# Optimization experiments

Hardware: AMD Instinct MI355X
Metric: run time of the kernel (lower is better)

## Reference

```python
import jax, jax.numpy as jnp
import numpy as np
import math

H, M, N = 64, 128, 128  # volume dims (m == n required by original index math)
K_NEIGH = 9
W_WIN = 3


def build_neighbor_ids(h, n, w):
    # Periodic (wrap-around) neighbor indices, matching extract_neighbour_indices
    # with m == n. Loop order: z-major, then y, then x, offsets -1..1 for w=3.
    half = w // 2
    offs = list(range(-half, half + 1))
    zi = jnp.arange(h)[:, None, None]
    yi = jnp.arange(n)[None, :, None]
    xi = jnp.arange(n)[None, None, :]
    cols = []
    for oz in offs:
        for oy in offs:
            for ox in offs:
                idx = ((zi + oz) % h) * (n * n) + ((yi + oy) % n) * n + ((xi + ox) % n)
                cols.append(idx.reshape(-1))
    return jnp.stack(cols, axis=1).astype(jnp.int32)  # [P, w^3]


def setup_inputs() -> dict:
    key = jax.random.key(0)
    k1, _ = jax.random.split(key)
    inp = jax.random.normal(k1, (H, M, N), dtype=jnp.float32)
    ksigma = jnp.ones((1, 1, 1, 1), dtype=jnp.float32)  # nn.Parameter init to sigma_m=1.0
    return {"input": inp, "ksigma": ksigma, "k": K_NEIGH, "w": W_WIN}


def reference(input, ksigma, k, w):
    h, m, n = input.shape
    ID = build_neighbor_ids(h, n, w)               # [P, nN]
    anat = input.reshape(-1)                       # [P]
    # get_knn: absolute intensity differences to each neighbor
    dist = jnp.abs(anat[ID] - anat[:, None])       # [P, nN]
    order = jnp.argsort(dist, axis=-1, stable=True)
    sID = jnp.take_along_axis(ID, order, axis=1)   # sorted neighbor indices
    IDk = sID[:, :k]                               # [P, k] top-k nearest by intensity
    Wk = anat[IDk]                                 # [P, k] neighbor intensities (feature rows)
    # get_features: per-row std (torch.std is unbiased, ddof=1)
    sigma = jnp.std(Wk, axis=1, ddof=1)            # [P]
    sigma_safe = jnp.where(sigma == 0, 1.0, sigma)
    neigh = Wk[IDk]                                # [P, k, k] gather feature rows of knn
    diff = Wk[:, None, :] - neigh + 1e-6           # pairwise_distance eps added to diff
    norm = jnp.sqrt(jnp.sum(diff * diff, axis=-1)) # [P, k] L2 pairwise distance
    ks = ksigma.reshape(())
    logits = -jnp.square(norm / sigma_safe[:, None] / (math.sqrt(2.0) * ks))
    logits = jnp.where(sigma[:, None] == 0, 0.0, logits)  # zero row -> uniform softmax
    Kw = jax.nn.softmax(logits, axis=1)            # [P, k] normalized kernel weights
    return Kw
```

## Files before the change

### kernel.cpp

```cpp
#include <hip/hip_runtime.h>
#include <hip/hip_fp16.h>
#include <array>

constexpr int HZ   = 64;
constexpr int NN   = 128;
constexpr int P    = HZ * NN * NN;
constexpr int KSEL = 9;
constexpr int NCOL = 27;

typedef _Float16 f16x2 __attribute__((ext_vector_type(2)));

constexpr int CZ = 4, CY = 8, CX = 32;
constexpr int RZ = 6, RY = 10, RX = 34;
constexpr int NROWS = RZ * RY * RX;
constexpr int IZ = 8, IY = 12, IXW = 40;
constexpr int NIN = IZ * IY * IXW;
constexpr int NIN16 = IZ * IY * (IXW / 4);

constexpr int compute_nce(int n) {
  int t = 0; while ((1 << t) < n) ++t;
  int cnt = 0;
  for (int p = 1 << (t - 1); p > 0; p >>= 1) {
    int q = 1 << (t - 1), r = 0, d = p;
    while (true) {
      for (int i = 0; i < n - d; ++i)
        if ((i & p) == r) ++cnt;
      if (q == p) break;
      d = q - p; r = p; q >>= 1;
    }
  }
  return cnt;
}
constexpr int NCE_FULL = compute_nce(NCOL);

struct CEPair { unsigned char a, b; };
constexpr std::array<CEPair, NCE_FULL> make_net() {
  std::array<CEPair, NCE_FULL> net{};
  int t = 0; while ((1 << t) < NCOL) ++t;
  int k = 0;
  for (int p = 1 << (t - 1); p > 0; p >>= 1) {
    int q = 1 << (t - 1), r = 0, d = p;
    while (true) {
      for (int i = 0; i < NCOL - d; ++i)
        if ((i & p) == r) {
          net[k].a = (unsigned char)i;
          net[k].b = (unsigned char)(i + d);
          ++k;
        }
      if (q == p) break;
      d = q - p; r = p; q >>= 1;
    }
  }
  return net;
}
constexpr auto FULLNET = make_net();

constexpr int count_pruned() {
  bool needed[NCOL] = {};
  for (int i = 0; i < KSEL; ++i) needed[i] = true;
  int cnt = 0;
  for (int e = NCE_FULL - 1; e >= 0; --e) {
    const int a = FULLNET[e].a, b = FULLNET[e].b;
    if (needed[a] || needed[b]) { needed[a] = true; needed[b] = true; ++cnt; }
  }
  return cnt;
}
constexpr int NCE = count_pruned();

constexpr std::array<CEPair, NCE> make_pruned() {
  bool needed[NCOL] = {};
  for (int i = 0; i < KSEL; ++i) needed[i] = true;
  std::array<bool, NCE_FULL> keep{};
  for (int e = NCE_FULL - 1; e >= 0; --e) {
    const int a = FULLNET[e].a, b = FULLNET[e].b;
    if (needed[a] || needed[b]) { keep[e] = true; needed[a] = true; needed[b] = true; }
  }
  std::array<CEPair, NCE> out{};
  int k = 0;
  for (int e = 0; e < NCE_FULL; ++e) if (keep[e]) out[k++] = FULLNET[e];
  return out;
}
constexpr auto NET = make_pruned();

typedef const __attribute__((address_space(1))) unsigned GU;
typedef __attribute__((address_space(3))) unsigned LU;

__device__ __forceinline__ void g2l16(const void* g, void* l) {
  __builtin_amdgcn_global_load_lds((GU*)g, (LU*)l, 16, 0, 0);
}

__global__ __launch_bounds__(512) void buildk_fused(
    const float* __restrict__ anat,
    const float* __restrict__ ksig,
    float* __restrict__ out) {
  __shared__ unsigned lds[NROWS * 6 + NIN];
  unsigned* tA  = lds;
  unsigned* tB0 = lds + NROWS * 4;
  unsigned* tB1 = tB0 + NROWS;
  float*    in_t = (float*)(tB1 + NROWS);

  const int tid = threadIdx.x;

  const int blk = blockIdx.x;
  const int swz = ((blk & 7) << 7) | (blk >> 3);
  const int zt   = swz >> 6;
  const int rest = swz & 63;
  const int y0   = ((rest >> 2) & 15) << 3;
  const int x0   = (rest & 3) << 5;
  const int z0   = zt << 2;

  #pragma unroll
  for (int s = 0; s < 2; ++s) {
    const unsigned q = (unsigned)(s * 512 + tid);
    if (q < (unsigned)NIN16) {
      const unsigned p = q / 10u;
      const unsigned t = q - 10u * p;
      const unsigned iz = p / 12u;
      const unsigned iy = p - 12u * iz;
      const int zz = (z0 + (int)iz - 2) & (HZ - 1);
      const int yy = (y0 + (int)iy - 2) & (NN - 1);
      const int xb = (x0 - 4 + 4 * (int)t) & (NN - 1);
      g2l16(&anat[(zz << 14) | (yy << 7) | xb], &in_t[q * 4]);
    }
  }
  __syncthreads();

  #pragma unroll 1
  for (int s = 0; s < 4; ++s) {
    const int r = s * 512 + tid;
    if (r < NROWS) {
      const unsigned ru = (unsigned)r;
      const unsigned rz  = ru / (unsigned)(RY * RX);
      const unsigned rem = ru - (unsigned)(RY * RX) * rz;
      const unsigned ry  = rem / (unsigned)RX;
      const unsigned rx  = rem - (unsigned)RX * ry;

      const float center = in_t[((rz + 1) * IY + (ry + 1)) * IXW + rx + 3];

      unsigned long long key[NCOL];
      #pragma unroll
      for (int c = 0; c < NCOL; ++c) {
        const int czi = c / 9, cyi = (c / 3) % 3, cxi = c % 3;
        const float v = in_t[((rz + czi) * IY + (ry + cyi)) * IXW + rx + cxi + 2];
        const unsigned vb = __float_as_uint(v);
        const unsigned db = __float_as_uint(v - center) & 0x7fffffffu;
        const unsigned lo32 = ((unsigned)c << 27) | (vb >> 5);
        key[c] = ((unsigned long long)db << 32) | lo32;
      }

      #pragma unroll
      for (int e = 0; e < NCE; ++e) {
        const int a = NET[e].a, b = NET[e].b;
        const double ka = __builtin_bit_cast(double, key[a]);
        const double kb = __builtin_bit_cast(double, key[b]);
        key[a] = __builtin_bit_cast(unsigned long long, fmin(ka, kb));
        key[b] = __builtin_bit_cast(unsigned long long, fmax(ka, kb));
      }

      unsigned od[4] = {0, 0, 0, 0};
      unsigned h8 = 0, lo = 0, hi = 0;
      #pragma unroll
      for (int k = 0; k < KSEL; ++k) {
        const unsigned kl = (unsigned)key[k];
        const unsigned c  = (kl >> 27) & 31u;
        const unsigned vbits = (kl & 0x07ffffffu) << 5;
        const unsigned hb = (unsigned)__half_as_ushort(__float2half(__uint_as_float(vbits)));
        if (k < 8) od[k >> 1] |= hb << ((k & 1) * 16);
        else       h8 = hb;
        if (k < 6) lo |= c << (5 * k);
        else       hi |= c << (5 * (k - 6));
      }

      *(uint4*)&tA[ru * 4] = make_uint4(od[0], od[1], od[2], od[3]);
      tB0[ru] = h8 | (hi << 16);
      tB1[ru] = lo;
    }
  }
  __syncthreads();

  const int xl = tid & 31;
  const int yl = (tid >> 5) & 7;
  const int zl = tid >> 8;

  const float ks = ksig[0];
  const _Float16 epsh = (_Float16)1e-6f;
  const f16x2 eps2 = {epsh, epsh};

  float res[2][9];

  #pragma unroll 2
  for (int vz = 0; vz < 2; ++vz) {
    const int zv = 2 * zl + vz;

    const int rho_own = ((zv + 1) * RY + (yl + 1)) * RX + (xl + 1);
    const uint4 a = *(const uint4*)&tA[rho_own * 4];
    const unsigned b0 = tB0[rho_own];
    const unsigned lo = tB1[rho_own];
    f16x2 wh[5];
    wh[0] = __builtin_bit_cast(f16x2, a.x);
    wh[1] = __builtin_bit_cast(f16x2, a.y);
    wh[2] = __builtin_bit_cast(f16x2, a.z);
    wh[3] = __builtin_bit_cast(f16x2, a.w);
    wh[4] = __builtin_bit_cast(f16x2, b0 & 0xffffu);
    const unsigned hi = b0 >> 16;

    int rho[KSEL];
    #pragma unroll
    for (int j = 0; j < KSEL; ++j) {
      const unsigned c = (j < 6) ? ((lo >> (5 * j)) & 31u)
                                 : ((hi >> (5 * (j - 6))) & 31u);
      const unsigned czi = (c * 57u) >> 9;
      const unsigned rem = c - 9u * czi;
      const unsigned cyi = (rem * 11u) >> 5;
      const unsigned cxi = rem - 3u * cyi;
      rho[j] = ((zv + (int)czi) * RY + (yl + (int)cyi)) * RX + (xl + (int)cxi);
    }
    uint4 na[KSEL];
    unsigned nb[KSEL];
    #pragma unroll
    for (int j = 0; j < KSEL; ++j) {
      na[j] = *(const uint4*)&tA[rho[j] * 4];
      nb[j] = tB0[rho[j]];
    }

    float ws[KSEL];
    #pragma unroll
    for (int l = 0; l < KSEL; ++l) ws[l] = (float)wh[l >> 1][l & 1];
    float mean = 0.f;
    #pragma unroll
    for (int l = 0; l < KSEL; ++l) mean += ws[l];
    mean *= (1.0f / 9.0f);
    float var = 0.f;
    #pragma unroll
    for (int l = 0; l < KSEL; ++l) { const float t = ws[l] - mean; var += t * t; }
    var *= (1.0f / 8.0f);
    const float sigma = sqrtf(var);

    const float inv2 = (sigma == 0.f)
        ? 0.f
        : 1.4426950408889634f / (2.0f * ks * ks * sigma * sigma);

    float logit[KSEL];
    #pragma unroll
    for (int j = 0; j < KSEL; ++j) {
      const f16x2 nh0 = __builtin_bit_cast(f16x2, na[j].x);
      const f16x2 nh1 = __builtin_bit_cast(f16x2, na[j].y);
      const f16x2 nh2 = __builtin_bit_cast(f16x2, na[j].z);
      const f16x2 nh3 = __builtin_bit_cast(f16x2, na[j].w);
      const f16x2 nh4 = __builtin_bit_cast(f16x2, nb[j] & 0xffffu);
      float s = 0.f;
      f16x2 dd;
      dd = (wh[0] - nh0) + eps2; s = __builtin_amdgcn_fdot2(dd, dd, s, false);
      dd = (wh[1] - nh1) + eps2; s = __builtin_amdgcn_fdot2(dd, dd, s, false);
      dd = (wh[2] - nh2) + eps2; s = __builtin_amdgcn_fdot2(dd, dd, s, false);
      dd = (wh[3] - nh3) + eps2; s = __builtin_amdgcn_fdot2(dd, dd, s, false);
      dd = (wh[4] - nh4) + eps2; s = __builtin_amdgcn_fdot2(dd, dd, s, false);
      logit[j] = -s * inv2;
    }

    float mx = logit[0];
    #pragma unroll
    for (int j = 1; j < KSEL; ++j) mx = fmaxf(mx, logit[j]);
    float sum = 0.f;
    float e[KSEL];
    #pragma unroll
    for (int j = 0; j < KSEL; ++j) { e[j] = exp2f(logit[j] - mx); sum += e[j]; }
    const float rs = 1.0f / sum;
    #pragma unroll
    for (int j = 0; j < KSEL; ++j) res[vz][j] = e[j] * rs;
  }

  __syncthreads();
  float* tf = (float*)lds;
  #pragma unroll 2
  for (int vz = 0; vz < 2; ++vz) {
    const int zv = 2 * zl + vz;
    const int pos = (zv << 8) + (yl << 5) + xl;
    #pragma unroll
    for (int j = 0; j < KSEL; ++j) tf[pos * KSEL + j] = res[vz][j];
  }
  __syncthreads();

  const float4* tf4 = (const float4*)lds;
  #pragma unroll
  for (int s = 0; s < 5; ++s) {
    const unsigned q = (unsigned)(s * 512 + tid);
    if (q < 2304u) {
      const unsigned row = q / 72u;
      const unsigned f   = q - row * 72u;
      const int zz = z0 + (int)(row >> 3);
      const int yr = (int)(row & 7u);
      const unsigned vb = (unsigned)((zz << 14) | ((y0 + yr) << 7) | x0);
      ((float4*)out)[(size_t)(vb >> 2) * 9 + f] = tf4[row * 72 + f];
    }
  }
}

extern "C" void kernel_launch(void* const* d_in, const int* in_sizes, int n_in,
                              void* d_out, int out_size, void* d_ws, size_t ws_size,
                              hipStream_t stream) {
  const float* anat = (const float*)d_in[0];
  const float* ksig = (const float*)d_in[1];
  buildk_fused<<<P / (CZ * CY * CX), 512, 0, stream>>>(anat, ksig, (float*)d_out);
}
```

Measured before the change: 105.8 us.

## Assign core rows to owning threads and keep their neighbor codes in registers

The sort phase is remapped so that each thread first sorts the two core rows it later consumes, then processes halo rows via a constexpr index table. The neighbor-code words (lo/hi) for core rows stay in registers instead of being written to and re-read from LDS, and the 9th-value half is stored as a 16-bit array. This shrinks LDS per block from roughly 6 words per row to 4.5, and launch_bounds(512,6) asks for higher occupancy. The trade-offs are a constant-memory halo table lookup, more divergent work in the halo passes, and register pressure under the tighter bound.

Result: slower. 118.0 us (+11.5%).

```diff
diff --git a/kernel.cpp b/kernel.cpp
--- a/kernel.cpp
+++ b/kernel.cpp
@@ -11,8 +11,10 @@
 typedef _Float16 f16x2 __attribute__((ext_vector_type(2)));
 
 constexpr int CZ = 4, CY = 8, CX = 32;
+constexpr int NCORE = CZ * CY * CX;
 constexpr int RZ = 6, RY = 10, RX = 34;
 constexpr int NROWS = RZ * RY * RX;
+constexpr int NHALO = NROWS - NCORE;
 constexpr int IZ = 8, IY = 12, IXW = 40;
 constexpr int NIN = IZ * IY * IXW;
 constexpr int NIN16 = IZ * IY * (IXW / 4);
@@ -82,6 +84,20 @@
 }
 constexpr auto NET = make_pruned();
 
+constexpr std::array<unsigned short, NHALO> make_halo() {
+  std::array<unsigned short, NHALO> t{};
+  int k = 0;
+  for (int r = 0; r < NROWS; ++r) {
+    const int rz = r / (RY * RX), rem = r % (RY * RX);
+    const int ry = rem / RX, rx = rem % RX;
+    const bool core = (rz >= 1 && rz <= CZ) && (ry >= 1 && ry <= CY) &&
+                      (rx >= 1 && rx <= CX);
+    if (!core) t[k++] = (unsigned short)r;
+  }
+  return t;
+}
+__device__ constexpr auto HALO = make_halo();
+
 typedef const __attribute__((address_space(1))) unsigned GU;
 typedef __attribute__((address_space(3))) unsigned LU;
 
@@ -89,15 +105,53 @@
   __builtin_amdgcn_global_load_lds((GU*)g, (LU*)l, 16, 0, 0);
 }
 
-__global__ __launch_bounds__(512) void buildk_fused(
+__device__ __forceinline__ void sort_row(
+    const float* __restrict__ in_t, int rz, int ry, int rx,
+    unsigned od[4], unsigned& h8, unsigned& lo, unsigned& hi) {
+  const float center = in_t[((rz + 1) * IY + (ry + 1)) * IXW + rx + 3];
+
+  unsigned long long key[NCOL];
+  #pragma unroll
+  for (int c = 0; c < NCOL; ++c) {
+    const int czi = c / 9, cyi = (c / 3) % 3, cxi = c % 3;
+    const float v = in_t[((rz + czi) * IY + (ry + cyi)) * IXW + rx + cxi + 2];
+    const unsigned vb = __float_as_uint(v);
+    const unsigned db = __float_as_uint(v - center) & 0x7fffffffu;
+    key[c] = ((unsigned long long)db << 32) |
+             (((unsigned)c << 27) | (vb >> 5));
+  }
+
+  #pragma unroll
+  for (int e = 0; e < NCE; ++e) {
+    const int a = NET[e].a, b = NET[e].b;
+    const double ka = __builtin_bit_cast(double, key[a]);
+    const double kb = __builtin_bit_cast(double, key[b]);
+    key[a] = __builtin_bit_cast(unsigned long long, fmin(ka, kb));
+    key[b] = __builtin_bit_cast(unsigned long long, fmax(ka, kb));
+  }
+
+  od[0] = od[1] = od[2] = od[3] = 0; h8 = 0; lo = 0; hi = 0;
+  #pragma unroll
+  for (int k = 0; k < KSEL; ++k) {
+    const unsigned kl = (unsigned)key[k];
+    const unsigned c  = (kl >> 27) & 31u;
+    const unsigned vbits = (kl & 0x07ffffffu) << 5;
+    const unsigned hb = (unsigned)__half_as_ushort(__float2half(__uint_as_float(vbits)));
+    if (k < 8) od[k >> 1] |= hb << ((k & 1) * 16);
+    else       h8 = hb;
+    if (k < 6) lo |= c << (5 * k);
+    else       hi |= c << (5 * (k - 6));
+  }
+}
+
+__global__ __launch_bounds__(512, 6) void buildk_fused2(
     const float* __restrict__ anat,
     const float* __restrict__ ksig,
     float* __restrict__ out) {
-  __shared__ unsigned lds[NROWS * 6 + NIN];
-  unsigned* tA  = lds;
-  unsigned* tB0 = lds + NROWS * 4;
-  unsigned* tB1 = tB0 + NROWS;
-  float*    in_t = (float*)(tB1 + NROWS);
+  __shared__ __align__(16) unsigned char ldsb[NROWS * 16 + NROWS * 2 + NIN * 4];
+  unsigned*       tA   = (unsigned*)ldsb;
+  unsigned short* tB0h = (unsigned short*)(ldsb + NROWS * 16);
+  float*          in_t = (float*)(ldsb + NROWS * 16 + NROWS * 2);
 
   const int tid = threadIdx.x;
 
@@ -108,6 +162,10 @@
   const int y0   = ((rest >> 2) & 15) << 3;
   const int x0   = (rest & 3) << 5;
   const int z0   = zt << 2;
+
+  const int xl = tid & 31;
+  const int yl = (tid >> 5) & 7;
+  const int zl = tid >> 8;
 
   #pragma unroll
   for (int s = 0; s < 2; ++s) {
@@ -125,62 +183,32 @@
   }
   __syncthreads();
 
+  unsigned lo0 = 0, hi0 = 0, lo1 = 0, hi1 = 0;
   #pragma unroll 1
   for (int s = 0; s < 4; ++s) {
-    const int r = s * 512 + tid;
-    if (r < NROWS) {
-      const unsigned ru = (unsigned)r;
-      const unsigned rz  = ru / (unsigned)(RY * RX);
-      const unsigned rem = ru - (unsigned)(RY * RX) * rz;
-      const unsigned ry  = rem / (unsigned)RX;
-      const unsigned rx  = rem - (unsigned)RX * ry;
-
-      const float center = in_t[((rz + 1) * IY + (ry + 1)) * IXW + rx + 3];
-
-      unsigned long long key[NCOL];
-      #pragma unroll
-      for (int c = 0; c < NCOL; ++c) {
-        const int czi = c / 9, cyi = (c / 3) % 3, cxi = c % 3;
-        const float v = in_t[((rz + czi) * IY + (ry + cyi)) * IXW + rx + cxi + 2];
-        const unsigned vb = __float_as_uint(v);
-        const unsigned db = __float_as_uint(v - center) & 0x7fffffffu;
-        const unsigned lo32 = ((unsigned)c << 27) | (vb >> 5);
-        key[c] = ((unsigned long long)db << 32) | lo32;
+    int rz = -1, ry = 0, rx = 0, ru = 0;
+    if (s < 2) {
+      rz = 2 * zl + s + 1; ry = yl + 1; rx = xl + 1;
+      ru = (rz * RY + ry) * RX + rx;
+    } else {
+      const int idx = (s - 2) * 512 + tid;
+      if (idx < NHALO) {
+        ru = (int)HALO[idx];
+        rz = ru / (RY * RX);
+        const int rem = ru - (RY * RX) * rz;
+        ry = rem / RX; rx = rem - RX * ry;
       }
-
-      #pragma unroll
-      for (int e = 0; e < NCE; ++e) {
-        const int a = NET[e].a, b = NET[e].b;
-        const double ka = __builtin_bit_cast(double, key[a]);
-        const double kb = __builtin_bit_cast(double, key[b]);
-        key[a] = __builtin_bit_cast(unsigned long long, fmin(ka, kb));
-        key[b] = __builtin_bit_cast(unsigned long long, fmax(ka, kb));
-      }
-
-      unsigned od[4] = {0, 0, 0, 0};
-      unsigned h8 = 0, lo = 0, hi = 0;
-      #pragma unroll
-      for (int k = 0; k < KSEL; ++k) {
-        const unsigned kl = (unsigned)key[k];
-        const unsigned c  = (kl >> 27) & 31u;
-        const unsigned vbits = (kl & 0x07ffffffu) << 5;
-        const unsigned hb = (unsigned)__half_as_ushort(__float2half(__uint_as_float(vbits)));
-        if (k < 8) od[k >> 1] |= hb << ((k & 1) * 16);
-        else       h8 = hb;
-        if (k < 6) lo |= c << (5 * k);
-        else       hi |= c << (5 * (k - 6));
-      }
-
-      *(uint4*)&tA[ru * 4] = make_uint4(od[0], od[1], od[2], od[3]);
-      tB0[ru] = h8 | (hi << 16);
-      tB1[ru] = lo;
+    }
+    if (rz >= 0) {
+      unsigned od[4], h8, lo, hi;
+      sort_row(in_t, rz, ry, rx, od, h8, lo, hi);
+      *(uint4*)&tA[(unsigned)ru * 4] = make_uint4(od[0], od[1], od[2], od[3]);
+      tB0h[ru] = (unsigned short)h8;
+      if (s == 0) { lo0 = lo; hi0 = hi; }
+      if (s == 1) { lo1 = lo; hi1 = hi; }
     }
   }
   __syncthreads();
-
-  const int xl = tid & 31;
-  const int yl = (tid >> 5) & 7;
-  const int zl = tid >> 8;
 
   const float ks = ksig[0];
   const _Float16 epsh = (_Float16)1e-6f;
@@ -188,21 +216,21 @@
 
   float res[2][9];
 
-  #pragma unroll 2
+  #pragma unroll
   for (int vz = 0; vz < 2; ++vz) {
     const int zv = 2 * zl + vz;
+    const unsigned lo = (vz == 0) ? lo0 : lo1;
+    const unsigned hi = (vz == 0) ? hi0 : hi1;
 
     const int rho_own = ((zv + 1) * RY + (yl + 1)) * RX + (xl + 1);
     const uint4 a = *(const uint4*)&tA[rho_own * 4];
-    const unsigned b0 = tB0[rho_own];
-    const unsigned lo = tB1[rho_own];
+    const unsigned b0 = (unsigned)tB0h[rho_own];
     f16x2 wh[5];
     wh[0] = __builtin_bit_cast(f16x2, a.x);
     wh[1] = __builtin_bit_cast(f16x2, a.y);
     wh[2] = __builtin_bit_cast(f16x2, a.z);
     wh[3] = __builtin_bit_cast(f16x2, a.w);
-    wh[4] = __builtin_bit_cast(f16x2, b0 & 0xffffu);
-    const unsigned hi = b0 >> 16;
+    wh[4] = __builtin_bit_cast(f16x2, b0);
 
     int rho[KSEL];
     #pragma unroll
@@ -220,7 +248,7 @@
     #pragma unroll
     for (int j = 0; j < KSEL; ++j) {
       na[j] = *(const uint4*)&tA[rho[j] * 4];
-      nb[j] = tB0[rho[j]];
+      nb[j] = (unsigned)tB0h[rho[j]];
     }
 
     float ws[KSEL];
@@ -247,7 +275,7 @@
       const f16x2 nh1 = __builtin_bit_cast(f16x2, na[j].y);
       const f16x2 nh2 = __builtin_bit_cast(f16x2, na[j].z);
       const f16x2 nh3 = __builtin_bit_cast(f16x2, na[j].w);
-      const f16x2 nh4 = __builtin_bit_cast(f16x2, nb[j] & 0xffffu);
+      const f16x2 nh4 = __builtin_bit_cast(f16x2, nb[j]);
       float s = 0.f;
       f16x2 dd;
       dd = (wh[0] - nh0) + eps2; s = __builtin_amdgcn_fdot2(dd, dd, s, false);
@@ -271,8 +299,8 @@
   }
 
   __syncthreads();
-  float* tf = (float*)lds;
-  #pragma unroll 2
+  float* tf = (float*)ldsb;
+  #pragma unroll
   for (int vz = 0; vz < 2; ++vz) {
     const int zv = 2 * zl + vz;
     const int pos = (zv << 8) + (yl << 5) + xl;
@@ -281,7 +309,7 @@
   }
   __syncthreads();
 
-  const float4* tf4 = (const float4*)lds;
+  const float4* tf4 = (const float4*)ldsb;
   #pragma unroll
   for (int s = 0; s < 5; ++s) {
     const unsigned q = (unsigned)(s * 512 + tid);
@@ -301,5 +329,5 @@
                               hipStream_t stream) {
   const float* anat = (const float*)d_in[0];
   const float* ksig = (const float*)d_in[1];
-  buildk_fused<<<P / (CZ * CY * CX), 512, 0, stream>>>(anat, ksig, (float*)d_out);
-}
+  buildk_fused2<<<P / NCORE, 512, 0, stream>>>(anat, ksig, (float*)d_out);
+}
```
